# Kernel optimization log

Measured on AMD Instinct MI355X. Metric: run time of the kernel, lower is better.

## Reference

```python
import jax, jax.numpy as jnp
import numpy as np
import math

B, S, D, H = 2, 2048, 1024, 16
DK = D // H


def setup_inputs() -> dict:
    key = jax.random.key(0)
    k1, k2, k3, k4, k5, k6 = jax.random.split(key, 6)
    scale = 1.0 / math.sqrt(D)
    return {
        "query": jax.random.normal(k1, (B, S, D), dtype=jnp.float32),
        "key": jax.random.normal(k2, (B, S, D), dtype=jnp.float32),
        "value": jax.random.normal(k3, (B, S, D), dtype=jnp.float32),
        "Wqkv": jax.random.normal(k4, (D, D), dtype=jnp.float32) * scale,
        "Wout": jax.random.normal(k5, (D, D), dtype=jnp.float32) * scale,
        "mask": jax.random.randint(k6, (B, 1, S, S), 0, 2, dtype=jnp.int32),
    }


def reference(query, key, value, Wqkv, Wout, mask):
    # Single shared QKV projection (same weight applied to q, k, v), no bias.
    q = query @ Wqkv.T
    k = key @ Wqkv.T
    v = value @ Wqkv.T
    # Faithful to the original: reshape (B, S, D) -> (B, H, S, DK) directly
    # (torch .reshape(n_batches, h, -1, d_k), NOT view+transpose).
    q = q.reshape(B, H, S, DK)
    k = k.reshape(B, H, S, DK)
    v = v.reshape(B, H, S, DK)
    scores = jnp.einsum("bhqd,bhkd->bhqk", q, k) / math.sqrt(DK)
    scores = jnp.where(mask == 0, jnp.float32(-1e9), scores)
    p_attn = jax.nn.softmax(scores, axis=-1)  # dropout is identity in eval
    x = jnp.einsum("bhqk,bhkd->bhqd", p_attn, v)  # [B,H,S,DK]
    x = x.transpose(0, 2, 1, 3).reshape(B, S, H * DK)
    return x @ Wout.T
```

## Files before the change

kernel.cpp:

```cpp
#include <hip/hip_runtime.h>
#include <stdint.h>


typedef __bf16 bf16;
typedef __bf16 bf16x8 __attribute__((ext_vector_type(8)));
typedef __bf16 bf16x4 __attribute__((ext_vector_type(4)));
typedef float f32x4 __attribute__((ext_vector_type(4)));

#define MFMA16(a, b, c) __builtin_amdgcn_mfma_f32_16x16x32_bf16((a), (b), (c), 0, 0, 0)
#define EXP2(x) __builtin_amdgcn_exp2f(x)

static constexpr int BATCH = 2;
static constexpr int SEQ = 2048;
static constexpr int DIM = 1024;
static constexpr int DK = 64;
static constexpr float QSCALE = 0.125f * 1.44269504088896340736f;

__device__ inline void gload16(const void* g, void* l) {
  __builtin_amdgcn_global_load_lds((const __attribute__((address_space(1))) void*)g,
                                   (__attribute__((address_space(3))) void*)l, 16, 0, 0);
}

__global__ __launch_bounds__(256) void mask_bits_kernel(const int* __restrict__ mask,
                                                        unsigned long long* __restrict__ bits) {
  int idx = blockIdx.x * 256 + threadIdx.x;
  int m = mask[idx];
  unsigned long long bal = __ballot(m != 0);
  if ((threadIdx.x & 63) == 0) bits[idx >> 6] = bal;
}

__global__ __launch_bounds__(256) void cvt_bf16_kernel(const float* __restrict__ s0,
                                                       const float* __restrict__ s1,
                                                       const float* __restrict__ s2,
                                                       const float* __restrict__ s3,
                                                       const float* __restrict__ s4,
                                                       bf16* __restrict__ d0, bf16* __restrict__ d1,
                                                       bf16* __restrict__ d2, bf16* __restrict__ d3,
                                                       bf16* __restrict__ d4) {
  const int y = blockIdx.y;
  const float* s = (y == 0) ? s0 : (y == 1) ? s1 : (y == 2) ? s2 : (y == 3) ? s3 : s4;
  bf16* d = (y == 0) ? d0 : (y == 1) ? d1 : (y == 2) ? d2 : (y == 3) ? d3 : d4;
  const int n8 = (y < 3) ? (BATCH * SEQ * DIM / 8) : (DIM * DIM / 8);
  for (int i = blockIdx.x * 256 + threadIdx.x; i < n8; i += gridDim.x * 256) {
    const float4 a = ((const float4*)s)[2 * i];
    const float4 b = ((const float4*)s)[2 * i + 1];
    bf16x8 v;
    v[0] = (bf16)a.x;
    v[1] = (bf16)a.y;
    v[2] = (bf16)a.z;
    v[3] = (bf16)a.w;
    v[4] = (bf16)b.x;
    v[5] = (bf16)b.y;
    v[6] = (bf16)b.z;
    v[7] = (bf16)b.w;
    ((bf16x8*)d)[i] = v;
  }
}

template <int BM, int NBY, int NBZ, typename TC>
__global__ __launch_bounds__(256, (BM == 128) ? 3 : 2) void gemm_bt_lds(
    const bf16* __restrict__ A0, const bf16* __restrict__ A1, const bf16* __restrict__ A2,
    const bf16* __restrict__ W, TC* __restrict__ C0, TC* __restrict__ C1, TC* __restrict__ C2,
    float scale0) {
  constexpr int K = 1024, N = 1024;
  constexpr int MT = BM / 32;
  constexpr int NB = 8 * NBY * NBZ;
  __shared__ __align__(16) bf16 As[2][BM * 32];
  __shared__ __align__(16) bf16 Bs[2][128 * 32];

  const int lin = blockIdx.x + 8 * (blockIdx.y + NBY * blockIdx.z);
  const int l = (lin & 7) * (NB / 8) + (lin >> 3);
  const int lx = l & 7;
  const int lyz = l >> 3;
  const int ly = lyz % NBY;
  const int lz = lyz / NBY;

  const bf16* A = (lz == 0) ? A0 : (lz == 1) ? A1 : A2;
  TC* C = (lz == 0) ? C0 : (lz == 1) ? C1 : C2;
  const float sc = (lz == 0) ? scale0 : 1.0f;

  const int tid = threadIdx.x;
  const int lane = tid & 63;
  const int wv = tid >> 6;
  const int wm = wv >> 1, wn = wv & 1;
  const int lrow = lane & 15, quad = lane >> 4;
  const int m0 = ly * BM, n0 = lx * 128;

  const int r0 = tid >> 2, c0 = (tid & 3) * 8;
  const bf16* pa0 = A + (size_t)(m0 + r0) * K + c0;
  const bf16* pb0 = W + (size_t)(n0 + r0) * K + c0;
  const bf16* pb1 = W + (size_t)(n0 + 64 + r0) * K + c0;
  const bf16* pa1 = nullptr;
  if constexpr (BM == 128) pa1 = A + (size_t)(m0 + 64 + r0) * K + c0;

  const f32x4 fz = {0.f, 0.f, 0.f, 0.f};
  f32x4 acc[MT][4];
#pragma unroll
  for (int i = 0; i < MT; ++i)
#pragma unroll
    for (int j = 0; j < 4; ++j) acc[i][j] = fz;

  gload16(pa0, &As[0][tid * 8]);
  if constexpr (BM == 128) gload16(pa1, &As[0][2048 + tid * 8]);
  gload16(pb0, &Bs[0][tid * 8]);
  gload16(pb1, &Bs[0][2048 + tid * 8]);
  __syncthreads();

  for (int t = 0; t < K / 32; ++t) {
    const int cur = t & 1;
    if (t + 1 < K / 32) {
      const int k1 = (t + 1) * 32;
      gload16(pa0 + k1, &As[cur ^ 1][tid * 8]);
      if constexpr (BM == 128) gload16(pa1 + k1, &As[cur ^ 1][2048 + tid * 8]);
      gload16(pb0 + k1, &Bs[cur ^ 1][tid * 8]);
      gload16(pb1 + k1, &Bs[cur ^ 1][2048 + tid * 8]);
    }
    bf16x8 af[MT], bfr[4];
#pragma unroll
    for (int mt = 0; mt < MT; ++mt)
      af[mt] = *(const bf16x8*)(&As[cur][(wm * (BM / 2) + mt * 16 + lrow) * 32 + quad * 8]);
#pragma unroll
    for (int nt = 0; nt < 4; ++nt)
      bfr[nt] = *(const bf16x8*)(&Bs[cur][(wn * 64 + nt * 16 + lrow) * 32 + quad * 8]);
#pragma unroll
    for (int mt = 0; mt < MT; ++mt)
#pragma unroll
      for (int nt = 0; nt < 4; ++nt) acc[mt][nt] = MFMA16(af[mt], bfr[nt], acc[mt][nt]);
    __syncthreads();
  }

#pragma unroll
  for (int mt = 0; mt < MT; ++mt) {
    const int gm = m0 + wm * (BM / 2) + mt * 16 + quad * 4;
#pragma unroll
    for (int nt = 0; nt < 4; ++nt) {
      const int gn = n0 + wn * 64 + nt * 16 + lrow;
#pragma unroll
      for (int r = 0; r < 4; ++r) C[(size_t)(gm + r) * N + gn] = (TC)(acc[mt][nt][r] * sc);
    }
  }
}

__global__ __launch_bounds__(256, 2) void attn_kernel(const bf16* __restrict__ Qg,
                                                      const bf16* __restrict__ Kg,
                                                      const bf16* __restrict__ Vg,
                                                      const unsigned* __restrict__ bits,
                                                      bf16* __restrict__ Y) {
  constexpr int LQ = 72;
  constexpr int LV = 66;
  __shared__ bf16 Qs[128 * LQ];
  __shared__ bf16 Ks[64 * LQ];
  __shared__ bf16 Vt0[64 * LV];
  __shared__ bf16 Vt1[64 * LV];
  __shared__ bf16 Ps[4][32 * LQ];

  const int tid = threadIdx.x;
  const int lane = tid & 63;
  const int wv = tid >> 6;
  const int lrow = lane & 15, quad = lane >> 4;
  const int bh = blockIdx.y;
  const int b = bh >> 4, h = bh & 15;
  const int q0 = blockIdx.x * 128;

  const bf16* Qh = Qg + (size_t)bh * (SEQ * DK);
  const bf16* Kh = Kg + (size_t)bh * (SEQ * DK);
  const bf16* Vh = Vg + (size_t)bh * (SEQ * DK);

#pragma unroll
  for (int i = 0; i < 4; ++i) {
    int s = tid + i * 256;
    int row = s >> 3, c8 = (s & 7) * 8;
    *(uint4*)(&Qs[row * LQ + c8]) = *(const uint4*)(Qh + (size_t)(q0 + row) * DK + c8);
  }

  const int krow = tid >> 3;
  const int kc8 = (tid & 7) * 8;
  const bf16* pk0 = Kh + (size_t)krow * DK + kc8;
  const bf16* pk1 = Kh + (size_t)(krow + 32) * DK + kc8;
  const int vn2 = tid & 31;
  const int vk2b = tid >> 5;
  const bf16* pv0 = Vh + (size_t)(vk2b + 0) * 2 * DK + vn2 * 2;
  const bf16* pv1 = Vh + (size_t)(vk2b + 8) * 2 * DK + vn2 * 2;
  const bf16* pv2 = Vh + (size_t)(vk2b + 16) * 2 * DK + vn2 * 2;
  const bf16* pv3 = Vh + (size_t)(vk2b + 24) * 2 * DK + vn2 * 2;

  uint4 kr0, kr1;
  uint32_t va[4], vb[4];

  kr0 = *(const uint4*)(pk0);
  kr1 = *(const uint4*)(pk1);
  va[0] = *(const uint32_t*)(pv0);
  vb[0] = *(const uint32_t*)(pv0 + DK);
  va[1] = *(const uint32_t*)(pv1);
  vb[1] = *(const uint32_t*)(pv1 + DK);
  va[2] = *(const uint32_t*)(pv2);
  vb[2] = *(const uint32_t*)(pv2 + DK);
  va[3] = *(const uint32_t*)(pv3);
  vb[3] = *(const uint32_t*)(pv3 + DK);
  *(uint4*)(&Ks[krow * LQ + kc8]) = kr0;
  *(uint4*)(&Ks[(krow + 32) * LQ + kc8]) = kr1;
#pragma unroll
  for (int i = 0; i < 4; ++i) {
    uint32_t t0 = (va[i] & 0xffffu) | (vb[i] << 16);
    uint32_t t1 = (va[i] >> 16) | (vb[i] & 0xffff0000u);
    *(uint32_t*)(&Vt0[(vn2 * 2) * LV + (vk2b + i * 8) * 2]) = t0;
    *(uint32_t*)(&Vt0[(vn2 * 2 + 1) * LV + (vk2b + i * 8) * 2]) = t1;
  }
  __syncthreads();

  bf16x8 qf[2][2];
#pragma unroll
  for (int nt = 0; nt < 2; ++nt)
#pragma unroll
    for (int ks = 0; ks < 2; ++ks)
      qf[nt][ks] = *(const bf16x8*)(&Qs[(wv * 32 + nt * 16 + lrow) * LQ + ks * 32 + quad * 8]);
  __syncthreads();

  const f32x4 fz = {0.f, 0.f, 0.f, 0.f};
  f32x4 of_t[4][2];
#pragma unroll
  for (int i = 0; i < 4; ++i)
#pragma unroll
    for (int j = 0; j < 2; ++j) of_t[i][j] = fz;
  float lsum[2] = {0.f, 0.f};

  const unsigned* bitrow = bits + (size_t)b * SEQ * (SEQ / 32);

  uint2 mwn[2];
#pragma unroll
  for (int nt = 0; nt < 2; ++nt) {
    int row = q0 + wv * 32 + nt * 16 + lrow;
    mwn[nt] = *(const uint2*)(bitrow + (size_t)row * (SEQ / 32));
  }

  for (int kt = 0; kt < 32; ++kt) {
    const int cur = kt & 1;
    bf16* kb = cur ? Qs : Ks;
    bf16* vbuf = cur ? Vt1 : Vt0;
    uint2 mwn_n[2];
    if (kt + 1 < 32) {
      const size_t adv = (size_t)(kt + 1) * 64 * DK;
      kr0 = *(const uint4*)(pk0 + adv);
      kr1 = *(const uint4*)(pk1 + adv);
      va[0] = *(const uint32_t*)(pv0 + adv);
      vb[0] = *(const uint32_t*)(pv0 + adv + DK);
      va[1] = *(const uint32_t*)(pv1 + adv);
      vb[1] = *(const uint32_t*)(pv1 + adv + DK);
      va[2] = *(const uint32_t*)(pv2 + adv);
      vb[2] = *(const uint32_t*)(pv2 + adv + DK);
      va[3] = *(const uint32_t*)(pv3 + adv);
      vb[3] = *(const uint32_t*)(pv3 + adv + DK);
#pragma unroll
      for (int nt = 0; nt < 2; ++nt) {
        int row = q0 + wv * 32 + nt * 16 + lrow;
        mwn_n[nt] = *(const uint2*)(bitrow + (size_t)row * (SEQ / 32) + (kt + 1) * 2);
      }
    }

    f32x4 st[4][2];
#pragma unroll
    for (int mt = 0; mt < 4; ++mt)
#pragma unroll
      for (int nt = 0; nt < 2; ++nt) st[mt][nt] = fz;
#pragma unroll
    for (int ks = 0; ks < 2; ++ks) {
#pragma unroll
      for (int mt = 0; mt < 4; ++mt) {
        bf16x8 kfv = *(const bf16x8*)(kb + (mt * 16 + lrow) * LQ + ks * 32 + quad * 8);
#pragma unroll
        for (int nt = 0; nt < 2; ++nt) st[mt][nt] = MFMA16(kfv, qf[nt][ks], st[mt][nt]);
      }
    }

#pragma unroll
    for (int nt = 0; nt < 2; ++nt) {
      uint32_t ux = mwn[nt].x >> (quad * 4);
      uint32_t uy = mwn[nt].y >> (quad * 4);
      float psum = 0.f;
#pragma unroll
      for (int mt = 0; mt < 4; ++mt) {
        uint32_t u = (mt & 2) ? uy : ux;
        int sh = (mt & 1) << 4;
        bf16x4 pk;
#pragma unroll
        for (int r = 0; r < 4; ++r) {
          float p = EXP2(st[mt][nt][r]);
          p = ((u >> (sh + r)) & 1u) ? p : 0.f;
          psum += p;
          pk[r] = (bf16)p;
        }
        *(bf16x4*)(&Ps[wv][(nt * 16 + lrow) * LQ + mt * 16 + quad * 4]) = pk;
      }
      lsum[nt] += psum;
    }

#pragma unroll
    for (int ks = 0; ks < 2; ++ks) {
      bf16x8 avf[4], bpf[2];
#pragma unroll
      for (int dkt = 0; dkt < 4; ++dkt)
        avf[dkt] = *(const bf16x8*)(vbuf + (dkt * 16 + lrow) * LV + ks * 32 + quad * 8);
#pragma unroll
      for (int rt = 0; rt < 2; ++rt)
        bpf[rt] = *(const bf16x8*)(&Ps[wv][(rt * 16 + lrow) * LQ + ks * 32 + quad * 8]);
#pragma unroll
      for (int dkt = 0; dkt < 4; ++dkt)
#pragma unroll
        for (int rt = 0; rt < 2; ++rt) of_t[dkt][rt] = MFMA16(avf[dkt], bpf[rt], of_t[dkt][rt]);
    }

    if (kt + 1 < 32) {
      bf16* kbn = cur ? Ks : Qs;
      bf16* vbn = cur ? Vt0 : Vt1;
      *(uint4*)(kbn + krow * LQ + kc8) = kr0;
      *(uint4*)(kbn + (krow + 32) * LQ + kc8) = kr1;
#pragma unroll
      for (int i = 0; i < 4; ++i) {
        uint32_t t0 = (va[i] & 0xffffu) | (vb[i] << 16);
        uint32_t t1 = (va[i] >> 16) | (vb[i] & 0xffff0000u);
        *(uint32_t*)(vbn + (vn2 * 2) * LV + (vk2b + i * 8) * 2) = t0;
        *(uint32_t*)(vbn + (vn2 * 2 + 1) * LV + (vk2b + i * 8) * 2) = t1;
      }
      mwn[0] = mwn_n[0];
      mwn[1] = mwn_n[1];
    }
    __syncthreads();
  }

  float linv[2];
#pragma unroll
  for (int nt = 0; nt < 2; ++nt) {
    float v = lsum[nt];
    v += __shfl_xor(v, 16);
    v += __shfl_xor(v, 32);
    linv[nt] = 1.0f / fmaxf(v, 1e-20f);
  }

#pragma unroll
  for (int dkt = 0; dkt < 4; ++dkt)
#pragma unroll
    for (int rt = 0; rt < 2; ++rt) {
      bf16x4 o;
#pragma unroll
      for (int j = 0; j < 4; ++j) o[j] = (bf16)(of_t[dkt][rt][j] * linv[rt]);
      const int row = q0 + wv * 32 + rt * 16 + lrow;
      *(bf16x4*)(&Y[((size_t)b * SEQ + row) * DIM + h * 64 + dkt * 16 + quad * 4]) = o;
    }
}

extern "C" void kernel_launch(void* const* d_in, const int* in_sizes, int n_in,
                              void* d_out, int out_size, void* d_ws, size_t ws_size,
                              hipStream_t stream) {
  const float* query = (const float*)d_in[0];
  const float* key = (const float*)d_in[1];
  const float* value = (const float*)d_in[2];
  const float* Wqkv = (const float*)d_in[3];
  const float* Wout = (const float*)d_in[4];
  const int* mask = (const int*)d_in[5];
  float* out = (float*)d_out;

  char* ws = (char*)d_ws;
  bf16* qin = (bf16*)(ws);
  bf16* kin = (bf16*)(ws + 8388608);
  bf16* vin = (bf16*)(ws + 16777216);
  bf16* Wq = (bf16*)(ws + 25165824);
  bf16* Wo = (bf16*)(ws + 27262976);
  bf16* q = (bf16*)(ws + 29360128);
  bf16* k = (bf16*)(ws + 37748736);
  bf16* v = (bf16*)(ws + 46137344);
  bf16* y = (bf16*)(ws);
  unsigned long long* bits64 = (unsigned long long*)(ws + 54525952);

  mask_bits_kernel<<<(BATCH * SEQ * SEQ) / 256, 256, 0, stream>>>(mask, bits64);

  cvt_bf16_kernel<<<dim3(256, 5), 256, 0, stream>>>(query, key, value, Wqkv, Wout,
                                                    qin, kin, vin, Wq, Wo);

  gemm_bt_lds<128, 32, 3, bf16>
      <<<dim3(8, 32, 3), 256, 0, stream>>>(qin, kin, vin, Wq, q, k, v, QSCALE);

  attn_kernel<<<dim3(16, 32), 256, 0, stream>>>(q, k, v, (const unsigned*)bits64, y);

  gemm_bt_lds<64, 64, 1, float>
      <<<dim3(8, 64, 1), 256, 0, stream>>>(y, y, y, Wo, out, out, out, 1.0f);
}
```

Before: 286.5 us.

## Swizzle GEMM LDS tiles, reuse Q buffer for V, load mask bits in-loop

The GEMM kernel now XOR-swizzles the 16-byte column chunk of each LDS row, both where global_load_lds writes it and where the MFMA operands are read, to cut LDS bank conflicts. The attention kernel drops its separate V double buffers: it keeps one V tile and reuses the upper half of the Q buffer as the second V buffer, with the row stride changed from 66 to 72. This lowers LDS use, which could allow more blocks per CU. The mask-bit words are now loaded within each iteration rather than prefetched a step ahead, which saves registers but exposes that load's latency.

Result: faster. 253.1 us (-11.7%).

```diff
diff --git a/kernel.cpp b/kernel.cpp
--- a/kernel.cpp
+++ b/kernel.cpp
@@ -86,7 +86,8 @@
   const int lrow = lane & 15, quad = lane >> 4;
   const int m0 = ly * BM, n0 = lx * 128;
 
-  const int r0 = tid >> 2, c0 = (tid & 3) * 8;
+  const int r0 = tid >> 2;
+  const int c0 = (((tid & 3) ^ ((r0 >> 1) & 3)) * 8);
   const bf16* pa0 = A + (size_t)(m0 + r0) * K + c0;
   const bf16* pb0 = W + (size_t)(n0 + r0) * K + c0;
   const bf16* pb1 = W + (size_t)(n0 + 64 + r0) * K + c0;
@@ -99,6 +100,9 @@
   for (int i = 0; i < MT; ++i)
 #pragma unroll
     for (int j = 0; j < 4; ++j) acc[i][j] = fz;
+
+  const int sw = (lrow >> 1) & 3;
+  const int rb = (quad ^ sw) * 8;
 
   gload16(pa0, &As[0][tid * 8]);
   if constexpr (BM == 128) gload16(pa1, &As[0][2048 + tid * 8]);
@@ -118,10 +122,10 @@
     bf16x8 af[MT], bfr[4];
 #pragma unroll
     for (int mt = 0; mt < MT; ++mt)
-      af[mt] = *(const bf16x8*)(&As[cur][(wm * (BM / 2) + mt * 16 + lrow) * 32 + quad * 8]);
+      af[mt] = *(const bf16x8*)(&As[cur][(wm * (BM / 2) + mt * 16 + lrow) * 32 + rb]);
 #pragma unroll
     for (int nt = 0; nt < 4; ++nt)
-      bfr[nt] = *(const bf16x8*)(&Bs[cur][(wn * 64 + nt * 16 + lrow) * 32 + quad * 8]);
+      bfr[nt] = *(const bf16x8*)(&Bs[cur][(wn * 64 + nt * 16 + lrow) * 32 + rb]);
 #pragma unroll
     for (int mt = 0; mt < MT; ++mt)
 #pragma unroll
@@ -147,11 +151,9 @@
                                                       const unsigned* __restrict__ bits,
                                                       bf16* __restrict__ Y) {
   constexpr int LQ = 72;
-  constexpr int LV = 66;
   __shared__ bf16 Qs[128 * LQ];
   __shared__ bf16 Ks[64 * LQ];
-  __shared__ bf16 Vt0[64 * LV];
-  __shared__ bf16 Vt1[64 * LV];
+  __shared__ bf16 Vts[64 * LQ];
   __shared__ bf16 Ps[4][32 * LQ];
 
   const int tid = threadIdx.x;
@@ -203,8 +205,8 @@
   for (int i = 0; i < 4; ++i) {
     uint32_t t0 = (va[i] & 0xffffu) | (vb[i] << 16);
     uint32_t t1 = (va[i] >> 16) | (vb[i] & 0xffff0000u);
-    *(uint32_t*)(&Vt0[(vn2 * 2) * LV + (vk2b + i * 8) * 2]) = t0;
-    *(uint32_t*)(&Vt0[(vn2 * 2 + 1) * LV + (vk2b + i * 8) * 2]) = t1;
+    *(uint32_t*)(&Vts[(vn2 * 2) * LQ + (vk2b + i * 8) * 2]) = t0;
+    *(uint32_t*)(&Vts[(vn2 * 2 + 1) * LQ + (vk2b + i * 8) * 2]) = t1;
   }
   __syncthreads();
 
@@ -226,18 +228,10 @@
 
   const unsigned* bitrow = bits + (size_t)b * SEQ * (SEQ / 32);
 
-  uint2 mwn[2];
-#pragma unroll
-  for (int nt = 0; nt < 2; ++nt) {
-    int row = q0 + wv * 32 + nt * 16 + lrow;
-    mwn[nt] = *(const uint2*)(bitrow + (size_t)row * (SEQ / 32));
-  }
-
   for (int kt = 0; kt < 32; ++kt) {
     const int cur = kt & 1;
     bf16* kb = cur ? Qs : Ks;
-    bf16* vbuf = cur ? Vt1 : Vt0;
-    uint2 mwn_n[2];
+    bf16* vbuf = cur ? (Qs + 64 * LQ) : Vts;
     if (kt + 1 < 32) {
       const size_t adv = (size_t)(kt + 1) * 64 * DK;
       kr0 = *(const uint4*)(pk0 + adv);
@@ -250,11 +244,12 @@
       vb[2] = *(const uint32_t*)(pv2 + adv + DK);
       va[3] = *(const uint32_t*)(pv3 + adv);
       vb[3] = *(const uint32_t*)(pv3 + adv + DK);
-#pragma unroll
-      for (int nt = 0; nt < 2; ++nt) {
-        int row = q0 + wv * 32 + nt * 16 + lrow;
-        mwn_n[nt] = *(const uint2*)(bitrow + (size_t)row * (SEQ / 32) + (kt + 1) * 2);
-      }
+    }
+    uint2 mwn[2];
+#pragma unroll
+    for (int nt = 0; nt < 2; ++nt) {
+      int row = q0 + wv * 32 + nt * 16 + lrow;
+      mwn[nt] = *(const uint2*)(bitrow + (size_t)row * (SEQ / 32) + kt * 2);
     }
 
     f32x4 st[4][2];
@@ -299,7 +294,7 @@
       bf16x8 avf[4], bpf[2];
 #pragma unroll
       for (int dkt = 0; dkt < 4; ++dkt)
-        avf[dkt] = *(const bf16x8*)(vbuf + (dkt * 16 + lrow) * LV + ks * 32 + quad * 8);
+        avf[dkt] = *(const bf16x8*)(vbuf + (dkt * 16 + lrow) * LQ + ks * 32 + quad * 8);
 #pragma unroll
       for (int rt = 0; rt < 2; ++rt)
         bpf[rt] = *(const bf16x8*)(&Ps[wv][(rt * 16 + lrow) * LQ + ks * 32 + quad * 8]);
@@ -311,18 +306,16 @@
 
     if (kt + 1 < 32) {
       bf16* kbn = cur ? Ks : Qs;
-      bf16* vbn = cur ? Vt0 : Vt1;
+      bf16* vbn = cur ? Vts : (Qs + 64 * LQ);
       *(uint4*)(kbn + krow * LQ + kc8) = kr0;
       *(uint4*)(kbn + (krow + 32) * LQ + kc8) = kr1;
 #pragma unroll
       for (int i = 0; i < 4; ++i) {
         uint32_t t0 = (va[i] & 0xffffu) | (vb[i] << 16);
         uint32_t t1 = (va[i] >> 16) | (vb[i] & 0xffff0000u);
-        *(uint32_t*)(vbn + (vn2 * 2) * LV + (vk2b + i * 8) * 2) = t0;
-        *(uint32_t*)(vbn + (vn2 * 2 + 1) * LV + (vk2b + i * 8) * 2) = t1;
+        *(uint32_t*)(vbn + (vn2 * 2) * LQ + (vk2b + i * 8) * 2) = t0;
+        *(uint32_t*)(vbn + (vn2 * 2 + 1) * LQ + (vk2b + i * 8) * 2) = t1;
       }
-      mwn[0] = mwn_n[0];
-      mwn[1] = mwn_n[1];
     }
     __syncthreads();
   }
```
